# Kernel optimization log

Hardware: AMD Instinct MI355X
Metric: run time of the kernel (lower is better)

## Reference

```python
import jax, jax.numpy as jnp
import numpy as np

RES = 128        # 2**base_lod, base_lod=7, num_lod=1
FEAT_DIM = 18


def setup_inputs() -> dict:
    key = jax.random.key(0)
    k1, k2 = jax.random.split(key)
    pts = jax.random.uniform(k1, (4, 524288, 3), dtype=jnp.float32)
    codebook = jax.random.normal(k2, (RES ** 3, FEAT_DIM), dtype=jnp.float32) * 0.01
    transform = jnp.eye(4, dtype=jnp.float32)
    return {"pts": pts, "codebook": codebook, "transform": transform}


def _trilinear(res, codebook, pts):
    # pts: [N,3] in [0,1]; NGLOD-style dense grid trilinear interpolation
    p = pts * (res - 1)
    p0 = jnp.floor(p)
    w = p - p0                                   # [N,3] fractional weights
    i0 = jnp.clip(p0.astype(jnp.int32), 0, res - 1)
    i1 = jnp.clip(i0 + 1, 0, res - 1)
    feats = jnp.zeros((pts.shape[0], codebook.shape[1]), dtype=codebook.dtype)
    for dz in (0, 1):
        iz = (i1 if dz else i0)[:, 2]
        wz = w[:, 2] if dz else 1.0 - w[:, 2]
        for dy in (0, 1):
            iy = (i1 if dy else i0)[:, 1]
            wy = w[:, 1] if dy else 1.0 - w[:, 1]
            for dx in (0, 1):
                ix = (i1 if dx else i0)[:, 0]
                wx = w[:, 0] if dx else 1.0 - w[:, 0]
                idx = ix + iy * res + iz * res * res   # x + y*res + z*res^2
                feats = feats + codebook[idx] * (wx * wy * wz)[:, None]
    return feats


def reference(pts, codebook, transform):
    # flatten 'b h c -> (b h) c'
    p = pts.reshape(-1, 3)
    R_inv = jnp.linalg.inv(transform[:3, :3])
    p = (R_inv @ (p.T - transform[:3, 3:4])).T
    feats = _trilinear(RES, codebook, p)
    # single LOD: cat over lod axis then sum(-1) is identity
    return feats
```

## Files before the change

### kernel.cpp

```cpp
#include <hip/hip_runtime.h>


constexpr int RES = 128;
constexpr int NB  = 512;
constexpr int TPB = 576;
constexpr int PPB = TPB / 9;

constexpr int HIST_CHUNK = 1024;
constexpr int SCAT_CHUNK = 4096;

typedef float vf2 __attribute__((ext_vector_type(2)));
typedef float vf4 __attribute__((ext_vector_type(4)));

struct Xf {
    float m00, m01, m02, m10, m11, m12, m20, m21, m22;
    float tx, ty, tz;
};

__device__ __forceinline__ Xf load_xf(const float* __restrict__ tr) {
    Xf X;
    const float a = tr[0], b = tr[1],  c = tr[2];
    const float d = tr[4], e = tr[5],  g = tr[6];
    const float h = tr[8], i = tr[9],  j = tr[10];
    X.tx = tr[3]; X.ty = tr[7]; X.tz = tr[11];
    const float det = a*(e*j - g*i) - b*(d*j - g*h) + c*(d*i - e*h);
    const float rd  = 1.0f / det;
    X.m00 = (e*j - g*i) * rd; X.m01 = (c*i - b*j) * rd; X.m02 = (b*g - c*e) * rd;
    X.m10 = (g*h - d*j) * rd; X.m11 = (a*j - c*h) * rd; X.m12 = (c*d - a*g) * rd;
    X.m20 = (d*i - e*h) * rd; X.m21 = (b*h - a*i) * rd; X.m22 = (a*e - b*d) * rd;
    return X;
}

__device__ __forceinline__ float qcoord(float m0, float m1, float m2,
                                        float x, float y, float z) {
    return __fmaf_rn(m0, x, __fmaf_rn(m1, y, m2 * z)) * (float)(RES - 1);
}

__device__ __forceinline__ int bin_of(const Xf& X, float x, float y, float z) {
    const float qy = qcoord(X.m10, X.m11, X.m12, x, y, z);
    const float qz = qcoord(X.m20, X.m21, X.m22, x, y, z);
    const int iy0 = min(max((int)floorf(qy), 0), RES - 1);
    const int iz0 = min(max((int)floorf(qz), 0), RES - 1);
    return (iz0 << 2) + (iy0 >> 5);
}

__global__ __launch_bounds__(NB)
void k_zero(unsigned* __restrict__ hist) {
    hist[threadIdx.x] = 0u;
}

__global__ __launch_bounds__(256)
void k_hist(const float* __restrict__ pts, const float* __restrict__ tr,
            unsigned* __restrict__ hist, int npts)
{
    __shared__ unsigned sh[NB];
    for (int b = threadIdx.x; b < NB; b += 256) sh[b] = 0u;
    __syncthreads();
    const Xf X = load_xf(tr);
    const int base = blockIdx.x * HIST_CHUNK;
    #pragma unroll
    for (int i = 0; i < HIST_CHUNK / 256; ++i) {
        const int p = base + threadIdx.x + i * 256;
        if (p < npts) {
            const float x = pts[p*3 + 0] - X.tx;
            const float y = pts[p*3 + 1] - X.ty;
            const float z = pts[p*3 + 2] - X.tz;
            atomicAdd(&sh[bin_of(X, x, y, z)], 1u);
        }
    }
    __syncthreads();
    for (int b = threadIdx.x; b < NB; b += 256) {
        const unsigned c = sh[b];
        if (c) atomicAdd(&hist[b], c);
    }
}

__global__ __launch_bounds__(NB)
void k_scan(const unsigned* __restrict__ hist, unsigned* __restrict__ cursor)
{
    __shared__ unsigned s[NB];
    const int t = threadIdx.x;
    const unsigned my = hist[t];
    s[t] = my;
    __syncthreads();
    for (int off = 1; off < NB; off <<= 1) {
        const unsigned v = (t >= off) ? s[t - off] : 0u;
        __syncthreads();
        s[t] += v;
        __syncthreads();
    }
    cursor[t] = s[t] - my;
}

__global__ __launch_bounds__(256)
void k_scatter(const float* __restrict__ pts, const float* __restrict__ tr,
               unsigned* __restrict__ cursor, vf4* __restrict__ rec, int npts)
{
    __shared__ unsigned shist[NB], sbase[NB], scur[NB];
    const int t = threadIdx.x;
    for (int b = t; b < NB; b += 256) { shist[b] = 0u; scur[b] = 0u; }
    __syncthreads();
    const Xf X = load_xf(tr);
    const int base = blockIdx.x * SCAT_CHUNK;
    #pragma unroll
    for (int i = 0; i < SCAT_CHUNK / 256; ++i) {
        const int p = base + t + i * 256;
        if (p < npts) {
            const float x = pts[p*3 + 0] - X.tx;
            const float y = pts[p*3 + 1] - X.ty;
            const float z = pts[p*3 + 2] - X.tz;
            atomicAdd(&shist[bin_of(X, x, y, z)], 1u);
        }
    }
    __syncthreads();
    for (int b = t; b < NB; b += 256)
        sbase[b] = atomicAdd(&cursor[b], shist[b]);
    __syncthreads();
    #pragma unroll
    for (int i = 0; i < SCAT_CHUNK / 256; ++i) {
        const int p = base + t + i * 256;
        if (p < npts) {
            const float x = pts[p*3 + 0] - X.tx;
            const float y = pts[p*3 + 1] - X.ty;
            const float z = pts[p*3 + 2] - X.tz;
            const float qx = qcoord(X.m00, X.m01, X.m02, x, y, z);
            const float qy = qcoord(X.m10, X.m11, X.m12, x, y, z);
            const float qz = qcoord(X.m20, X.m21, X.m22, x, y, z);
            const int bn = bin_of(X, x, y, z);
            const unsigned r = atomicAdd(&scur[bn], 1u);
            unsigned pos = sbase[bn] + r;
            if (pos >= (unsigned)npts) pos = (unsigned)npts - 1u;
            vf4 v; v.x = qx; v.y = qy; v.z = qz; v.w = __int_as_float(p);
            rec[pos] = v;
        }
    }
}

__global__ __launch_bounds__(TPB)
void k_main(const vf4* __restrict__ rec, const float* __restrict__ cb,
            float* __restrict__ out, int npts)
{
    __shared__ vf4 srec[PPB];
    if (threadIdx.x < PPB) {
        const int g = blockIdx.x * PPB + threadIdx.x;
        if (g < npts) srec[threadIdx.x] = rec[g];
    }
    __syncthreads();

    const int pl = threadIdx.x / 9;
    const int f  = threadIdx.x - pl * 9;
    const int p  = blockIdx.x * PPB + pl;
    if (p >= npts) return;

    const vf4 r = srec[pl];
    const float qx = r.x, qy = r.y, qz = r.z;
    const int idx = __float_as_int(r.w);

    const float fx = floorf(qx), fy = floorf(qy), fz = floorf(qz);
    const float wx1 = qx - fx, wy1 = qy - fy, wz1 = qz - fz;
    const float wx0 = 1.0f - wx1, wy0 = 1.0f - wy1, wz0 = 1.0f - wz1;
    const int ix0 = min(max((int)fx, 0), RES - 1); const int ix1 = min(ix0 + 1, RES - 1);
    const int iy0 = min(max((int)fy, 0), RES - 1); const int iy1 = min(iy0 + 1, RES - 1);
    const int iz0 = min(max((int)fz, 0), RES - 1); const int iz1 = min(iz0 + 1, RES - 1);

    int   ro[8];
    float w[8];
    #pragma unroll
    for (int k = 0; k < 8; ++k) {
        const int dx = k & 1, dy = (k >> 1) & 1, dz = k >> 2;
        const int ix = dx ? ix1 : ix0;
        const int iy = dy ? iy1 : iy0;
        const int iz = dz ? iz1 : iz0;
        ro[k] = ix + (iy << 7) + (iz << 14);
        w[k]  = (dx ? wx1 : wx0) * (dy ? wy1 : wy0) * (dz ? wz1 : wz0);
    }

    const float* cbf = cb + 2 * f;
    vf2 v[8];
    #pragma unroll
    for (int k = 0; k < 8; ++k)
        v[k] = *reinterpret_cast<const vf2*>(cbf + ro[k] * 18);

    float ax = 0.0f, ay = 0.0f;
    #pragma unroll
    for (int k = 0; k < 8; ++k) { ax += v[k].x * w[k]; ay += v[k].y * w[k]; }

    vf2 o; o.x = ax; o.y = ay;
    __builtin_nontemporal_store(o, reinterpret_cast<vf2*>(out + idx * 18 + 2 * f));
}

__global__ __launch_bounds__(TPB)
void dense_grid_trilerp(const float* __restrict__ pts,
                        const float* __restrict__ cb,
                        const float* __restrict__ tr,
                        float* __restrict__ out,
                        int npts)
{
    __shared__ float spts[PPB * 3];
    if (threadIdx.x < PPB * 3) {
        int g = blockIdx.x * (PPB * 3) + threadIdx.x;
        spts[threadIdx.x] = (g < npts * 3) ? __builtin_nontemporal_load(&pts[g]) : 0.0f;
    }
    __syncthreads();

    const int pl = threadIdx.x / 9;
    const int f  = threadIdx.x - pl * 9;
    const int p  = blockIdx.x * PPB + pl;
    if (p >= npts) return;

    const Xf X = load_xf(tr);
    const float x = spts[pl*3 + 0] - X.tx;
    const float y = spts[pl*3 + 1] - X.ty;
    const float z = spts[pl*3 + 2] - X.tz;
    const float qx = qcoord(X.m00, X.m01, X.m02, x, y, z);
    const float qy = qcoord(X.m10, X.m11, X.m12, x, y, z);
    const float qz = qcoord(X.m20, X.m21, X.m22, x, y, z);

    const float fx = floorf(qx), fy = floorf(qy), fz = floorf(qz);
    const float wx1 = qx - fx, wy1 = qy - fy, wz1 = qz - fz;
    const float wx0 = 1.0f - wx1, wy0 = 1.0f - wy1, wz0 = 1.0f - wz1;
    const int ix0 = min(max((int)fx, 0), RES - 1); const int ix1 = min(ix0 + 1, RES - 1);
    const int iy0 = min(max((int)fy, 0), RES - 1); const int iy1 = min(iy0 + 1, RES - 1);
    const int iz0 = min(max((int)fz, 0), RES - 1); const int iz1 = min(iz0 + 1, RES - 1);

    int   ro[8];
    float w[8];
    #pragma unroll
    for (int k = 0; k < 8; ++k) {
        const int dx = k & 1, dy = (k >> 1) & 1, dz = k >> 2;
        const int ix = dx ? ix1 : ix0;
        const int iy = dy ? iy1 : iy0;
        const int iz = dz ? iz1 : iz0;
        ro[k] = ix + (iy << 7) + (iz << 14);
        w[k]  = (dx ? wx1 : wx0) * (dy ? wy1 : wy0) * (dz ? wz1 : wz0);
    }

    const float* cbf = cb + 2 * f;
    vf2 v[8];
    #pragma unroll
    for (int k = 0; k < 8; ++k)
        v[k] = *reinterpret_cast<const vf2*>(cbf + ro[k] * 18);

    float ax = 0.0f, ay = 0.0f;
    #pragma unroll
    for (int k = 0; k < 8; ++k) { ax += v[k].x * w[k]; ay += v[k].y * w[k]; }

    vf2 o; o.x = ax; o.y = ay;
    __builtin_nontemporal_store(o, reinterpret_cast<vf2*>(out + p * 18 + 2 * f));
}

extern "C" void kernel_launch(void* const* d_in, const int* in_sizes, int n_in,
                              void* d_out, int out_size, void* d_ws, size_t ws_size,
                              hipStream_t stream) {
    const float* pts = (const float*)d_in[0];
    const float* cb  = (const float*)d_in[1];
    const float* tr  = (const float*)d_in[2];
    float* out = (float*)d_out;

    const int npts = in_sizes[0] / 3;

    const size_t need = (size_t)NB * 2 * sizeof(unsigned) + (size_t)npts * 16 + 256;
    if (d_ws == nullptr || ws_size < need || npts <= 0) {
        const int blocks = (npts + PPB - 1) / PPB;
        dense_grid_trilerp<<<blocks, TPB, 0, stream>>>(pts, cb, tr, out, npts);
        return;
    }

    unsigned* hist   = (unsigned*)d_ws;
    unsigned* cursor = hist + NB;
    vf4* rec = (vf4*)((char*)d_ws + ((size_t)NB * 2 * sizeof(unsigned) + 255) / 256 * 256);

    k_zero<<<1, NB, 0, stream>>>(hist);
    k_hist<<<(npts + HIST_CHUNK - 1) / HIST_CHUNK, 256, 0, stream>>>(pts, tr, hist, npts);
    k_scan<<<1, NB, 0, stream>>>(hist, cursor);
    k_scatter<<<(npts + SCAT_CHUNK - 1) / SCAT_CHUNK, 256, 0, stream>>>(pts, tr, cursor, rec, npts);
    k_main<<<(npts + PPB - 1) / PPB, TPB, 0, stream>>>(rec, cb, out, npts);
}
```

Measured before the change: 506.5 us.

## Bin points per (y,z) row pair and stage codebook rows in LDS

Points are now sorted into 16384 bins, one per (iy0, iz0) cell column, using global atomics for the histogram and scatter instead of per-block shared-memory histograms. A multi-chunk single-block scan builds the bin offsets. The main kernel runs one block per bin and loads the four needed codebook x-rows (128 by 18 floats each) into LDS once. Each point's eight corner fetches are then served from LDS rather than from global memory. The costs are heavy contention on global atomics, a serial scan over 16K bins, and load imbalance, since each block copies about 37 KB of LDS for roughly 32 points on average.

```diff
diff --git a/kernel.cpp b/kernel.cpp
--- a/kernel.cpp
+++ b/kernel.cpp
@@ -2,12 +2,10 @@
 
 
 constexpr int RES = 128;
-constexpr int NB  = 512;
+constexpr int NB2 = 128 * 128;
 constexpr int TPB = 576;
 constexpr int PPB = TPB / 9;
-
-constexpr int HIST_CHUNK = 1024;
-constexpr int SCAT_CHUNK = 4096;
+constexpr int ROWF = 128 * 18;
 
 typedef float vf2 __attribute__((ext_vector_type(2)));
 typedef float vf4 __attribute__((ext_vector_type(4)));
@@ -36,114 +34,164 @@
     return __fmaf_rn(m0, x, __fmaf_rn(m1, y, m2 * z)) * (float)(RES - 1);
 }
 
-__device__ __forceinline__ int bin_of(const Xf& X, float x, float y, float z) {
-    const float qy = qcoord(X.m10, X.m11, X.m12, x, y, z);
-    const float qz = qcoord(X.m20, X.m21, X.m22, x, y, z);
+__device__ __forceinline__ int bin_of_qyz(float qy, float qz) {
     const int iy0 = min(max((int)floorf(qy), 0), RES - 1);
     const int iz0 = min(max((int)floorf(qz), 0), RES - 1);
-    return (iz0 << 2) + (iy0 >> 5);
-}
-
-__global__ __launch_bounds__(NB)
+    return (iz0 << 7) | iy0;
+}
+
+__global__ __launch_bounds__(256)
 void k_zero(unsigned* __restrict__ hist) {
-    hist[threadIdx.x] = 0u;
+    const int i = blockIdx.x * 256 + threadIdx.x;
+    if (i < NB2) hist[i] = 0u;
 }
 
 __global__ __launch_bounds__(256)
 void k_hist(const float* __restrict__ pts, const float* __restrict__ tr,
             unsigned* __restrict__ hist, int npts)
 {
-    __shared__ unsigned sh[NB];
-    for (int b = threadIdx.x; b < NB; b += 256) sh[b] = 0u;
-    __syncthreads();
+    const int p = blockIdx.x * 256 + threadIdx.x;
+    if (p >= npts) return;
     const Xf X = load_xf(tr);
-    const int base = blockIdx.x * HIST_CHUNK;
-    #pragma unroll
-    for (int i = 0; i < HIST_CHUNK / 256; ++i) {
-        const int p = base + threadIdx.x + i * 256;
-        if (p < npts) {
-            const float x = pts[p*3 + 0] - X.tx;
-            const float y = pts[p*3 + 1] - X.ty;
-            const float z = pts[p*3 + 2] - X.tz;
-            atomicAdd(&sh[bin_of(X, x, y, z)], 1u);
+    const float x = pts[p*3 + 0] - X.tx;
+    const float y = pts[p*3 + 1] - X.ty;
+    const float z = pts[p*3 + 2] - X.tz;
+    const float qy = qcoord(X.m10, X.m11, X.m12, x, y, z);
+    const float qz = qcoord(X.m20, X.m21, X.m22, x, y, z);
+    atomicAdd(&hist[bin_of_qyz(qy, qz)], 1u);
+}
+
+__global__ __launch_bounds__(1024)
+void k_scan(const unsigned* __restrict__ hist,
+            unsigned* __restrict__ base, unsigned* __restrict__ cursor)
+{
+    __shared__ unsigned s[1024];
+    const int t = threadIdx.x;
+    unsigned carry = 0u;
+    for (int c = 0; c < NB2 / 1024; ++c) {
+        const int i = c * 1024 + t;
+        const unsigned v = hist[i];
+        s[t] = v;
+        __syncthreads();
+        for (int off = 1; off < 1024; off <<= 1) {
+            const unsigned tmp = (t >= off) ? s[t - off] : 0u;
+            __syncthreads();
+            s[t] += tmp;
+            __syncthreads();
         }
-    }
-    __syncthreads();
-    for (int b = threadIdx.x; b < NB; b += 256) {
-        const unsigned c = sh[b];
-        if (c) atomicAdd(&hist[b], c);
-    }
-}
-
-__global__ __launch_bounds__(NB)
-void k_scan(const unsigned* __restrict__ hist, unsigned* __restrict__ cursor)
-{
-    __shared__ unsigned s[NB];
-    const int t = threadIdx.x;
-    const unsigned my = hist[t];
-    s[t] = my;
-    __syncthreads();
-    for (int off = 1; off < NB; off <<= 1) {
-        const unsigned v = (t >= off) ? s[t - off] : 0u;
-        __syncthreads();
-        s[t] += v;
-        __syncthreads();
-    }
-    cursor[t] = s[t] - my;
+        const unsigned excl = s[t] - v + carry;
+        base[i]   = excl;
+        cursor[i] = excl;
+        const unsigned tot = s[1023];
+        __syncthreads();
+        carry += tot;
+    }
 }
 
 __global__ __launch_bounds__(256)
 void k_scatter(const float* __restrict__ pts, const float* __restrict__ tr,
                unsigned* __restrict__ cursor, vf4* __restrict__ rec, int npts)
 {
-    __shared__ unsigned shist[NB], sbase[NB], scur[NB];
+    const int p = blockIdx.x * 256 + threadIdx.x;
+    if (p >= npts) return;
+    const Xf X = load_xf(tr);
+    const float x = pts[p*3 + 0] - X.tx;
+    const float y = pts[p*3 + 1] - X.ty;
+    const float z = pts[p*3 + 2] - X.tz;
+    const float qx = qcoord(X.m00, X.m01, X.m02, x, y, z);
+    const float qy = qcoord(X.m10, X.m11, X.m12, x, y, z);
+    const float qz = qcoord(X.m20, X.m21, X.m22, x, y, z);
+    const int bn = bin_of_qyz(qy, qz);
+    unsigned pos = atomicAdd(&cursor[bn], 1u);
+    if (pos >= (unsigned)npts) pos = (unsigned)npts - 1u;
+    vf4 v; v.x = qx; v.y = qy; v.z = qz; v.w = __int_as_float(p);
+    rec[pos] = v;
+}
+
+__global__ __launch_bounds__(TPB)
+void k_main(const vf4* __restrict__ rec, const unsigned* __restrict__ hist,
+            const unsigned* __restrict__ base, const float* __restrict__ cb,
+            float* __restrict__ out)
+{
+    const int b = blockIdx.x;
+    const unsigned n = hist[b];
+    if (n == 0u) return;
+    const unsigned bs = base[b];
+
+    const int iy0 = b & 127, iz0 = b >> 7;
+    const int iy1 = min(iy0 + 1, RES - 1), iz1 = min(iz0 + 1, RES - 1);
+
+    __shared__ float sld[4 * ROWF];
+    __shared__ vf4   srec[PPB];
+
     const int t = threadIdx.x;
-    for (int b = t; b < NB; b += 256) { shist[b] = 0u; scur[b] = 0u; }
-    __syncthreads();
-    const Xf X = load_xf(tr);
-    const int base = blockIdx.x * SCAT_CHUNK;
-    #pragma unroll
-    for (int i = 0; i < SCAT_CHUNK / 256; ++i) {
-        const int p = base + t + i * 256;
-        if (p < npts) {
-            const float x = pts[p*3 + 0] - X.tx;
-            const float y = pts[p*3 + 1] - X.ty;
-            const float z = pts[p*3 + 2] - X.tz;
-            atomicAdd(&shist[bin_of(X, x, y, z)], 1u);
+    {
+        const int ry[4] = { iy0, iy1, iy0, iy1 };
+        const int rz[4] = { iz0, iz0, iz1, iz1 };
+        #pragma unroll
+        for (int c = 0; c < 4; ++c) {
+            const vf4* src =
+                reinterpret_cast<const vf4*>(cb + (size_t)((rz[c] << 14) | (ry[c] << 7)) * 18);
+            reinterpret_cast<vf4*>(&sld[c * ROWF])[t] = src[t];
         }
     }
-    __syncthreads();
-    for (int b = t; b < NB; b += 256)
-        sbase[b] = atomicAdd(&cursor[b], shist[b]);
-    __syncthreads();
-    #pragma unroll
-    for (int i = 0; i < SCAT_CHUNK / 256; ++i) {
-        const int p = base + t + i * 256;
-        if (p < npts) {
-            const float x = pts[p*3 + 0] - X.tx;
-            const float y = pts[p*3 + 1] - X.ty;
-            const float z = pts[p*3 + 2] - X.tz;
-            const float qx = qcoord(X.m00, X.m01, X.m02, x, y, z);
-            const float qy = qcoord(X.m10, X.m11, X.m12, x, y, z);
-            const float qz = qcoord(X.m20, X.m21, X.m22, x, y, z);
-            const int bn = bin_of(X, x, y, z);
-            const unsigned r = atomicAdd(&scur[bn], 1u);
-            unsigned pos = sbase[bn] + r;
-            if (pos >= (unsigned)npts) pos = (unsigned)npts - 1u;
-            vf4 v; v.x = qx; v.y = qy; v.z = qz; v.w = __int_as_float(p);
-            rec[pos] = v;
+
+    const int pl = t / 9;
+    const int f  = t - pl * 9;
+
+    for (unsigned off = 0; off < n; off += PPB) {
+        __syncthreads();
+        if (t < PPB && off + (unsigned)t < n)
+            srec[t] = rec[bs + off + (unsigned)t];
+        __syncthreads();
+
+        if (off + (unsigned)pl < n) {
+            const vf4 r = srec[pl];
+            const float qx = r.x, qy = r.y, qz = r.z;
+            const int idx = __float_as_int(r.w);
+
+            const float fx = floorf(qx), fy = floorf(qy), fz = floorf(qz);
+            const float wx1 = qx - fx, wy1 = qy - fy, wz1 = qz - fz;
+            const float wx0 = 1.0f - wx1, wy0 = 1.0f - wy1, wz0 = 1.0f - wz1;
+            const int ix0 = min(max((int)fx, 0), RES - 1);
+            const int ix1 = min(ix0 + 1, RES - 1);
+
+            const int x18_0 = ix0 * 18 + 2 * f;
+            const int x18_1 = ix1 * 18 + 2 * f;
+
+            vf2   v[8];
+            float w[8];
+            #pragma unroll
+            for (int k = 0; k < 8; ++k) {
+                const int dx = k & 1, dy = (k >> 1) & 1, dz = k >> 2;
+                const int cell = dy + 2 * dz;
+                const int o = cell * ROWF + (dx ? x18_1 : x18_0);
+                v[k] = *reinterpret_cast<const vf2*>(&sld[o]);
+                w[k] = (dx ? wx1 : wx0) * (dy ? wy1 : wy0) * (dz ? wz1 : wz0);
+            }
+
+            float ax = 0.0f, ay = 0.0f;
+            #pragma unroll
+            for (int k = 0; k < 8; ++k) { ax += v[k].x * w[k]; ay += v[k].y * w[k]; }
+
+            vf2 o2; o2.x = ax; o2.y = ay;
+            __builtin_nontemporal_store(o2,
+                reinterpret_cast<vf2*>(out + (size_t)idx * 18 + 2 * f));
         }
     }
 }
 
 __global__ __launch_bounds__(TPB)
-void k_main(const vf4* __restrict__ rec, const float* __restrict__ cb,
-            float* __restrict__ out, int npts)
-{
-    __shared__ vf4 srec[PPB];
-    if (threadIdx.x < PPB) {
-        const int g = blockIdx.x * PPB + threadIdx.x;
-        if (g < npts) srec[threadIdx.x] = rec[g];
+void dense_grid_trilerp(const float* __restrict__ pts,
+                        const float* __restrict__ cb,
+                        const float* __restrict__ tr,
+                        float* __restrict__ out,
+                        int npts)
+{
+    __shared__ float spts[PPB * 3];
+    if (threadIdx.x < PPB * 3) {
+        int g = blockIdx.x * (PPB * 3) + threadIdx.x;
+        spts[threadIdx.x] = (g < npts * 3) ? __builtin_nontemporal_load(&pts[g]) : 0.0f;
     }
     __syncthreads();
 
@@ -152,9 +200,13 @@
     const int p  = blockIdx.x * PPB + pl;
     if (p >= npts) return;
 
-    const vf4 r = srec[pl];
-    const float qx = r.x, qy = r.y, qz = r.z;
-    const int idx = __float_as_int(r.w);
+    const Xf X = load_xf(tr);
+    const float x = spts[pl*3 + 0] - X.tx;
+    const float y = spts[pl*3 + 1] - X.ty;
+    const float z = spts[pl*3 + 2] - X.tz;
+    const float qx = qcoord(X.m00, X.m01, X.m02, x, y, z);
+    const float qy = qcoord(X.m10, X.m11, X.m12, x, y, z);
+    const float qz = qcoord(X.m20, X.m21, X.m22, x, y, z);
 
     const float fx = floorf(qx), fy = floorf(qy), fz = floorf(qz);
     const float wx1 = qx - fx, wy1 = qy - fy, wz1 = qz - fz;
@@ -186,66 +238,6 @@
     for (int k = 0; k < 8; ++k) { ax += v[k].x * w[k]; ay += v[k].y * w[k]; }
 
     vf2 o; o.x = ax; o.y = ay;
-    __builtin_nontemporal_store(o, reinterpret_cast<vf2*>(out + idx * 18 + 2 * f));
-}
-
-__global__ __launch_bounds__(TPB)
-void dense_grid_trilerp(const float* __restrict__ pts,
-                        const float* __restrict__ cb,
-                        const float* __restrict__ tr,
-                        float* __restrict__ out,
-                        int npts)
-{
-    __shared__ float spts[PPB * 3];
-    if (threadIdx.x < PPB * 3) {
-        int g = blockIdx.x * (PPB * 3) + threadIdx.x;
-        spts[threadIdx.x] = (g < npts * 3) ? __builtin_nontemporal_load(&pts[g]) : 0.0f;
-    }
-    __syncthreads();
-
-    const int pl = threadIdx.x / 9;
-    const int f  = threadIdx.x - pl * 9;
-    const int p  = blockIdx.x * PPB + pl;
-    if (p >= npts) return;
-
-    const Xf X = load_xf(tr);
-    const float x = spts[pl*3 + 0] - X.tx;
-    const float y = spts[pl*3 + 1] - X.ty;
-    const float z = spts[pl*3 + 2] - X.tz;
-    const float qx = qcoord(X.m00, X.m01, X.m02, x, y, z);
-    const float qy = qcoord(X.m10, X.m11, X.m12, x, y, z);
-    const float qz = qcoord(X.m20, X.m21, X.m22, x, y, z);
-
-    const float fx = floorf(qx), fy = floorf(qy), fz = floorf(qz);
-    const float wx1 = qx - fx, wy1 = qy - fy, wz1 = qz - fz;
-    const float wx0 = 1.0f - wx1, wy0 = 1.0f - wy1, wz0 = 1.0f - wz1;
-    const int ix0 = min(max((int)fx, 0), RES - 1); const int ix1 = min(ix0 + 1, RES - 1);
-    const int iy0 = min(max((int)fy, 0), RES - 1); const int iy1 = min(iy0 + 1, RES - 1);
-    const int iz0 = min(max((int)fz, 0), RES - 1); const int iz1 = min(iz0 + 1, RES - 1);
-
-    int   ro[8];
-    float w[8];
-    #pragma unroll
-    for (int k = 0; k < 8; ++k) {
-        const int dx = k & 1, dy = (k >> 1) & 1, dz = k >> 2;
-        const int ix = dx ? ix1 : ix0;
-        const int iy = dy ? iy1 : iy0;
-        const int iz = dz ? iz1 : iz0;
-        ro[k] = ix + (iy << 7) + (iz << 14);
-        w[k]  = (dx ? wx1 : wx0) * (dy ? wy1 : wy0) * (dz ? wz1 : wz0);
-    }
-
-    const float* cbf = cb + 2 * f;
-    vf2 v[8];
-    #pragma unroll
-    for (int k = 0; k < 8; ++k)
-        v[k] = *reinterpret_cast<const vf2*>(cbf + ro[k] * 18);
-
-    float ax = 0.0f, ay = 0.0f;
-    #pragma unroll
-    for (int k = 0; k < 8; ++k) { ax += v[k].x * w[k]; ay += v[k].y * w[k]; }
-
-    vf2 o; o.x = ax; o.y = ay;
     __builtin_nontemporal_store(o, reinterpret_cast<vf2*>(out + p * 18 + 2 * f));
 }
 
@@ -259,7 +251,8 @@
 
     const int npts = in_sizes[0] / 3;
 
-    const size_t need = (size_t)NB * 2 * sizeof(unsigned) + (size_t)npts * 16 + 256;
+    const size_t meta  = (size_t)NB2 * 3 * sizeof(unsigned);
+    const size_t need  = meta + (size_t)npts * 16 + 256;
     if (d_ws == nullptr || ws_size < need || npts <= 0) {
         const int blocks = (npts + PPB - 1) / PPB;
         dense_grid_trilerp<<<blocks, TPB, 0, stream>>>(pts, cb, tr, out, npts);
@@ -267,12 +260,14 @@
     }
 
     unsigned* hist   = (unsigned*)d_ws;
-    unsigned* cursor = hist + NB;
-    vf4* rec = (vf4*)((char*)d_ws + ((size_t)NB * 2 * sizeof(unsigned) + 255) / 256 * 256);
-
-    k_zero<<<1, NB, 0, stream>>>(hist);
-    k_hist<<<(npts + HIST_CHUNK - 1) / HIST_CHUNK, 256, 0, stream>>>(pts, tr, hist, npts);
-    k_scan<<<1, NB, 0, stream>>>(hist, cursor);
-    k_scatter<<<(npts + SCAT_CHUNK - 1) / SCAT_CHUNK, 256, 0, stream>>>(pts, tr, cursor, rec, npts);
-    k_main<<<(npts + PPB - 1) / PPB, TPB, 0, stream>>>(rec, cb, out, npts);
-}
+    unsigned* base   = hist + NB2;
+    unsigned* cursor = base + NB2;
+    vf4* rec = (vf4*)((char*)d_ws + ((meta + 255) / 256) * 256);
+
+    const int pblocks = (npts + 255) / 256;
+    k_zero<<<(NB2 + 255) / 256, 256, 0, stream>>>(hist);
+    k_hist<<<pblocks, 256, 0, stream>>>(pts, tr, hist, npts);
+    k_scan<<<1, 1024, 0, stream>>>(hist, base, cursor);
+    k_scatter<<<pblocks, 256, 0, stream>>>(pts, tr, cursor, rec, npts);
+    k_main<<<NB2, TPB, 0, stream>>>(rec, hist, base, cb, out);
+}
```

Result: slower. 629.5 us (+24.3%).

## Sub-sort points by y row and stage codebook rows in LDS per coarse bin

Applied to the files above, without the earlier changes.

Adds a per-coarse-bin subsort kernel that reorders the binned point records by their y row. The main kernel now runs one block per (z, y-group) bin and streams the needed codebook rows for z and z+1 into a 4-slot LDS ring, so the 8-corner lookups read LDS instead of gathering from global memory. This is meant to cut the scattered global codebook reads. In exchange it adds an extra read/write pass over the records, a large LDS footprint that limits occupancy, a barrier per y row, and a slow global-gather fallback for bins with more than 8160 points.

```diff
diff --git a/kernel.cpp b/kernel.cpp
--- a/kernel.cpp
+++ b/kernel.cpp
@@ -1,13 +1,15 @@
 #include <hip/hip_runtime.h>
 
 
-constexpr int RES = 128;
-constexpr int NB  = 512;
-constexpr int TPB = 576;
-constexpr int PPB = TPB / 9;
+constexpr int RES  = 128;
+constexpr int NBA  = 512;
+constexpr int TPM  = 576;
+constexpr int PPB  = 64;
+constexpr int ROWF = 128 * 18;
+constexpr int SUB_CAP = 8160;
 
 constexpr int HIST_CHUNK = 1024;
-constexpr int SCAT_CHUNK = 4096;
+constexpr int SCAT_CHUNK = 8192;
 
 typedef float vf2 __attribute__((ext_vector_type(2)));
 typedef float vf4 __attribute__((ext_vector_type(4)));
@@ -36,69 +38,75 @@
     return __fmaf_rn(m0, x, __fmaf_rn(m1, y, m2 * z)) * (float)(RES - 1);
 }
 
-__device__ __forceinline__ int bin_of(const Xf& X, float x, float y, float z) {
-    const float qy = qcoord(X.m10, X.m11, X.m12, x, y, z);
-    const float qz = qcoord(X.m20, X.m21, X.m22, x, y, z);
-    const int iy0 = min(max((int)floorf(qy), 0), RES - 1);
-    const int iz0 = min(max((int)floorf(qz), 0), RES - 1);
-    return (iz0 << 2) + (iy0 >> 5);
-}
-
-__global__ __launch_bounds__(NB)
-void k_zero(unsigned* __restrict__ hist) {
-    hist[threadIdx.x] = 0u;
+__device__ __forceinline__ int clamp_idx(float q) {
+    return min(max((int)floorf(q), 0), RES - 1);
+}
+
+__device__ __forceinline__ int coarse_key(float qy, float qz) {
+    return (clamp_idx(qz) << 2) | (clamp_idx(qy) >> 5);
 }
 
 __global__ __launch_bounds__(256)
-void k_hist(const float* __restrict__ pts, const float* __restrict__ tr,
-            unsigned* __restrict__ hist, int npts)
-{
-    __shared__ unsigned sh[NB];
-    for (int b = threadIdx.x; b < NB; b += 256) sh[b] = 0u;
+void k_zero(unsigned* __restrict__ histA) {
+    const int i = blockIdx.x * 256 + threadIdx.x;
+    if (i < NBA) histA[i] = 0u;
+}
+
+__global__ __launch_bounds__(256)
+void k_histA(const float* __restrict__ pts, const float* __restrict__ tr,
+             unsigned* __restrict__ histA, int npts)
+{
+    __shared__ unsigned sh[NBA];
+    const int t = threadIdx.x;
+    for (int b = t; b < NBA; b += 256) sh[b] = 0u;
     __syncthreads();
     const Xf X = load_xf(tr);
     const int base = blockIdx.x * HIST_CHUNK;
     #pragma unroll
     for (int i = 0; i < HIST_CHUNK / 256; ++i) {
-        const int p = base + threadIdx.x + i * 256;
+        const int p = base + t + i * 256;
         if (p < npts) {
             const float x = pts[p*3 + 0] - X.tx;
             const float y = pts[p*3 + 1] - X.ty;
             const float z = pts[p*3 + 2] - X.tz;
-            atomicAdd(&sh[bin_of(X, x, y, z)], 1u);
-        }
-    }
-    __syncthreads();
-    for (int b = threadIdx.x; b < NB; b += 256) {
+            const float qy = qcoord(X.m10, X.m11, X.m12, x, y, z);
+            const float qz = qcoord(X.m20, X.m21, X.m22, x, y, z);
+            atomicAdd(&sh[coarse_key(qy, qz)], 1u);
+        }
+    }
+    __syncthreads();
+    for (int b = t; b < NBA; b += 256) {
         const unsigned c = sh[b];
-        if (c) atomicAdd(&hist[b], c);
-    }
-}
-
-__global__ __launch_bounds__(NB)
-void k_scan(const unsigned* __restrict__ hist, unsigned* __restrict__ cursor)
-{
-    __shared__ unsigned s[NB];
-    const int t = threadIdx.x;
-    const unsigned my = hist[t];
+        if (c) atomicAdd(&histA[b], c);
+    }
+}
+
+__global__ __launch_bounds__(NBA)
+void k_scanA(const unsigned* __restrict__ histA,
+             unsigned* __restrict__ baseA, unsigned* __restrict__ cursorA)
+{
+    __shared__ unsigned s[NBA];
+    const int t = threadIdx.x;
+    const unsigned my = histA[t];
     s[t] = my;
     __syncthreads();
-    for (int off = 1; off < NB; off <<= 1) {
+    for (int off = 1; off < NBA; off <<= 1) {
         const unsigned v = (t >= off) ? s[t - off] : 0u;
         __syncthreads();
         s[t] += v;
         __syncthreads();
     }
-    cursor[t] = s[t] - my;
+    baseA[t]   = s[t] - my;
+    cursorA[t] = s[t] - my;
 }
 
 __global__ __launch_bounds__(256)
-void k_scatter(const float* __restrict__ pts, const float* __restrict__ tr,
-               unsigned* __restrict__ cursor, vf4* __restrict__ rec, int npts)
-{
-    __shared__ unsigned shist[NB], sbase[NB], scur[NB];
-    const int t = threadIdx.x;
-    for (int b = t; b < NB; b += 256) { shist[b] = 0u; scur[b] = 0u; }
+void k_scatA(const float* __restrict__ pts, const float* __restrict__ tr,
+             unsigned* __restrict__ cursorA, vf4* __restrict__ rec, int npts)
+{
+    __shared__ unsigned shist[NBA], sbase[NBA], scur[NBA];
+    const int t = threadIdx.x;
+    for (int b = t; b < NBA; b += 256) { shist[b] = 0u; scur[b] = 0u; }
     __syncthreads();
     const Xf X = load_xf(tr);
     const int base = blockIdx.x * SCAT_CHUNK;
@@ -109,12 +117,14 @@
             const float x = pts[p*3 + 0] - X.tx;
             const float y = pts[p*3 + 1] - X.ty;
             const float z = pts[p*3 + 2] - X.tz;
-            atomicAdd(&shist[bin_of(X, x, y, z)], 1u);
-        }
-    }
-    __syncthreads();
-    for (int b = t; b < NB; b += 256)
-        sbase[b] = atomicAdd(&cursor[b], shist[b]);
+            const float qy = qcoord(X.m10, X.m11, X.m12, x, y, z);
+            const float qz = qcoord(X.m20, X.m21, X.m22, x, y, z);
+            atomicAdd(&shist[coarse_key(qy, qz)], 1u);
+        }
+    }
+    __syncthreads();
+    for (int b = t; b < NBA; b += 256)
+        sbase[b] = shist[b] ? atomicAdd(&cursorA[b], shist[b]) : 0u;
     __syncthreads();
     #pragma unroll
     for (int i = 0; i < SCAT_CHUNK / 256; ++i) {
@@ -126,7 +136,7 @@
             const float qx = qcoord(X.m00, X.m01, X.m02, x, y, z);
             const float qy = qcoord(X.m10, X.m11, X.m12, x, y, z);
             const float qz = qcoord(X.m20, X.m21, X.m22, x, y, z);
-            const int bn = bin_of(X, x, y, z);
+            const int bn = coarse_key(qy, qz);
             const unsigned r = atomicAdd(&scur[bn], 1u);
             unsigned pos = sbase[bn] + r;
             if (pos >= (unsigned)npts) pos = (unsigned)npts - 1u;
@@ -136,60 +146,159 @@
     }
 }
 
-__global__ __launch_bounds__(TPB)
-void k_main(const vf4* __restrict__ rec, const float* __restrict__ cb,
-            float* __restrict__ out, int npts)
-{
-    __shared__ vf4 srec[PPB];
-    if (threadIdx.x < PPB) {
-        const int g = blockIdx.x * PPB + threadIdx.x;
-        if (g < npts) srec[threadIdx.x] = rec[g];
-    }
-    __syncthreads();
-
-    const int pl = threadIdx.x / 9;
-    const int f  = threadIdx.x - pl * 9;
-    const int p  = blockIdx.x * PPB + pl;
-    if (p >= npts) return;
-
-    const vf4 r = srec[pl];
-    const float qx = r.x, qy = r.y, qz = r.z;
-    const int idx = __float_as_int(r.w);
-
-    const float fx = floorf(qx), fy = floorf(qy), fz = floorf(qz);
-    const float wx1 = qx - fx, wy1 = qy - fy, wz1 = qz - fz;
-    const float wx0 = 1.0f - wx1, wy0 = 1.0f - wy1, wz0 = 1.0f - wz1;
-    const int ix0 = min(max((int)fx, 0), RES - 1); const int ix1 = min(ix0 + 1, RES - 1);
-    const int iy0 = min(max((int)fy, 0), RES - 1); const int iy1 = min(iy0 + 1, RES - 1);
-    const int iz0 = min(max((int)fz, 0), RES - 1); const int iz1 = min(iz0 + 1, RES - 1);
-
-    int   ro[8];
-    float w[8];
-    #pragma unroll
-    for (int k = 0; k < 8; ++k) {
-        const int dx = k & 1, dy = (k >> 1) & 1, dz = k >> 2;
-        const int ix = dx ? ix1 : ix0;
-        const int iy = dy ? iy1 : iy0;
-        const int iz = dz ? iz1 : iz0;
-        ro[k] = ix + (iy << 7) + (iz << 14);
-        w[k]  = (dx ? wx1 : wx0) * (dy ? wy1 : wy0) * (dz ? wz1 : wz0);
-    }
-
-    const float* cbf = cb + 2 * f;
-    vf2 v[8];
-    #pragma unroll
-    for (int k = 0; k < 8; ++k)
-        v[k] = *reinterpret_cast<const vf2*>(cbf + ro[k] * 18);
-
-    float ax = 0.0f, ay = 0.0f;
-    #pragma unroll
-    for (int k = 0; k < 8; ++k) { ax += v[k].x * w[k]; ay += v[k].y * w[k]; }
-
-    vf2 o; o.x = ax; o.y = ay;
-    __builtin_nontemporal_store(o, reinterpret_cast<vf2*>(out + idx * 18 + 2 * f));
-}
-
-__global__ __launch_bounds__(TPB)
+__global__ __launch_bounds__(1024)
+void k_subsort(vf4* __restrict__ rec, const unsigned* __restrict__ histA,
+               const unsigned* __restrict__ baseA, unsigned* __restrict__ histF)
+{
+    const int cbn = blockIdx.x;
+    const int t = threadIdx.x;
+    const unsigned n = histA[cbn];
+    const unsigned b0 = baseA[cbn];
+    const int iz0 = cbn >> 2;
+    const int ybase = (cbn & 3) << 5;
+    const int bf = (iz0 << 7) | ybase;
+
+    if (n == 0u) { if (t < 32) histF[bf + t] = 0u; return; }
+    if (n > (unsigned)SUB_CAP) {
+        if (t < 32) histF[bf + t] = (t == 0) ? (n | 0x80000000u) : 0u;
+        return;
+    }
+
+    __shared__ vf4 c[SUB_CAP];
+    __shared__ unsigned h[32], cur[32];
+    if (t < 32) h[t] = 0u;
+    __syncthreads();
+
+    for (unsigned i = t; i < n; i += 1024) {
+        const vf4 v = rec[b0 + i];
+        c[i] = v;
+        const int key = min(max(clamp_idx(v.y) - ybase, 0), 31);
+        atomicAdd(&h[key], 1u);
+    }
+    __syncthreads();
+    if (t == 0) {
+        unsigned run = 0u;
+        for (int k = 0; k < 32; ++k) { cur[k] = run; run += h[k]; }
+    }
+    __syncthreads();
+    for (unsigned i = t; i < n; i += 1024) {
+        const vf4 v = c[i];
+        const int key = min(max(clamp_idx(v.y) - ybase, 0), 31);
+        const unsigned pos = atomicAdd(&cur[key], 1u);
+        rec[b0 + pos] = v;
+    }
+    if (t < 32) histF[bf + t] = h[t];
+}
+
+__global__ __launch_bounds__(TPM)
+void k_main5(const vf4* __restrict__ rec, const unsigned* __restrict__ histF,
+             const unsigned* __restrict__ baseA, const float* __restrict__ cbk,
+             float* __restrict__ out)
+{
+    const int blk = blockIdx.x;
+    const int iz0 = blk >> 2;
+    const int ybase = (blk & 3) << 5;
+    const int t = threadIdx.x;
+    const int pl = t / 9;
+    const int f  = t - pl * 9;
+
+    __shared__ float sld[4][2][ROWF];
+
+    const unsigned bs = baseA[blk];
+    const unsigned nj0raw = histF[(iz0 << 7) | ybase];
+
+    auto stage = [&](int yn) {
+        const int yc = min(yn, RES - 1);
+        const int s  = yn & 3;
+        #pragma unroll
+        for (int zz = 0; zz < 2; ++zz) {
+            const int zc = min(iz0 + zz, RES - 1);
+            const vf2* __restrict__ src =
+                reinterpret_cast<const vf2*>(cbk + (size_t)((zc << 14) | (yc << 7)) * 18);
+            vf2* dst = reinterpret_cast<vf2*>(&sld[s][zz][0]);
+            dst[t]       = src[t];
+            dst[t + TPM] = src[t + TPM];
+        }
+    };
+
+    if (nj0raw & 0x80000000u) {
+        const unsigned n = nj0raw & 0x7fffffffu;
+        for (unsigned off = 0; off < n; off += PPB) {
+            const unsigned pi = off + (unsigned)pl;
+            if (pi < n) {
+                const vf4 r = rec[bs + pi];
+                const float qx = r.x, qy = r.y, qz = r.z;
+                const int idx = __float_as_int(r.w);
+                const float fx = floorf(qx), fy = floorf(qy), fz = floorf(qz);
+                const float wx1 = qx - fx, wy1 = qy - fy, wz1 = qz - fz;
+                const float wx0 = 1.0f - wx1, wy0 = 1.0f - wy1, wz0 = 1.0f - wz1;
+                const int ix0 = clamp_idx(qx), ix1 = min(ix0 + 1, RES - 1);
+                const int iy0 = clamp_idx(qy), iy1 = min(iy0 + 1, RES - 1);
+                const int izp = clamp_idx(qz), iz1 = min(izp + 1, RES - 1);
+                vf2 v[8]; float w[8];
+                #pragma unroll
+                for (int k = 0; k < 8; ++k) {
+                    const int dx = k & 1, dy = (k >> 1) & 1, dz = k >> 2;
+                    const int ro = (dx ? ix1 : ix0) + ((dy ? iy1 : iy0) << 7)
+                                 + ((dz ? iz1 : izp) << 14);
+                    v[k] = *reinterpret_cast<const vf2*>(cbk + (size_t)ro * 18 + 2 * f);
+                    w[k] = (dx ? wx1 : wx0) * (dy ? wy1 : wy0) * (dz ? wz1 : wz0);
+                }
+                float ax = 0.0f, ay = 0.0f;
+                #pragma unroll
+                for (int k = 0; k < 8; ++k) { ax += v[k].x * w[k]; ay += v[k].y * w[k]; }
+                vf2 o; o.x = ax; o.y = ay;
+                __builtin_nontemporal_store(o,
+                    reinterpret_cast<vf2*>(out + (size_t)idx * 18 + 2 * f));
+            }
+        }
+        return;
+    }
+
+    stage(ybase);
+    stage(ybase + 1);
+    unsigned cur = bs;
+    __syncthreads();
+
+    for (int j = 0; j < 32; ++j) {
+        const int iy0 = ybase + j;
+        const unsigned nj = histF[(iz0 << 7) | iy0];
+        if (j < 31) stage(iy0 + 2);
+
+        const int sy0 = iy0 & 3, sy1 = (iy0 + 1) & 3;
+        for (unsigned off = 0; off < nj; off += PPB) {
+            const unsigned pi = off + (unsigned)pl;
+            if (pi < nj) {
+                const vf4 r = __builtin_nontemporal_load(&rec[cur + pi]);
+                const float qx = r.x, qy = r.y, qz = r.z;
+                const int idx = __float_as_int(r.w);
+                const float fx = floorf(qx), fy = floorf(qy), fz = floorf(qz);
+                const float wx1 = qx - fx, wy1 = qy - fy, wz1 = qz - fz;
+                const float wx0 = 1.0f - wx1, wy0 = 1.0f - wy1, wz0 = 1.0f - wz1;
+                const int ix0 = clamp_idx(qx), ix1 = min(ix0 + 1, RES - 1);
+                const int x0 = ix0 * 18 + 2 * f, x1 = ix1 * 18 + 2 * f;
+                vf2 v[8]; float w[8];
+                #pragma unroll
+                for (int k = 0; k < 8; ++k) {
+                    const int dx = k & 1, dy = (k >> 1) & 1, dz = k >> 2;
+                    const float* base_ = &sld[dy ? sy1 : sy0][dz][0];
+                    v[k] = *reinterpret_cast<const vf2*>(&base_[dx ? x1 : x0]);
+                    w[k] = (dx ? wx1 : wx0) * (dy ? wy1 : wy0) * (dz ? wz1 : wz0);
+                }
+                float ax = 0.0f, ay = 0.0f;
+                #pragma unroll
+                for (int k = 0; k < 8; ++k) { ax += v[k].x * w[k]; ay += v[k].y * w[k]; }
+                vf2 o; o.x = ax; o.y = ay;
+                __builtin_nontemporal_store(o,
+                    reinterpret_cast<vf2*>(out + (size_t)idx * 18 + 2 * f));
+            }
+        }
+        cur += nj;
+        __syncthreads();
+    }
+}
+
+__global__ __launch_bounds__(TPM)
 void dense_grid_trilerp(const float* __restrict__ pts,
                         const float* __restrict__ cb,
                         const float* __restrict__ tr,
@@ -219,19 +328,16 @@
     const float fx = floorf(qx), fy = floorf(qy), fz = floorf(qz);
     const float wx1 = qx - fx, wy1 = qy - fy, wz1 = qz - fz;
     const float wx0 = 1.0f - wx1, wy0 = 1.0f - wy1, wz0 = 1.0f - wz1;
-    const int ix0 = min(max((int)fx, 0), RES - 1); const int ix1 = min(ix0 + 1, RES - 1);
-    const int iy0 = min(max((int)fy, 0), RES - 1); const int iy1 = min(iy0 + 1, RES - 1);
-    const int iz0 = min(max((int)fz, 0), RES - 1); const int iz1 = min(iz0 + 1, RES - 1);
+    const int ix0 = clamp_idx(qx); const int ix1 = min(ix0 + 1, RES - 1);
+    const int iy0 = clamp_idx(qy); const int iy1 = min(iy0 + 1, RES - 1);
+    const int iz0 = clamp_idx(qz); const int iz1 = min(iz0 + 1, RES - 1);
 
     int   ro[8];
     float w[8];
     #pragma unroll
     for (int k = 0; k < 8; ++k) {
         const int dx = k & 1, dy = (k >> 1) & 1, dz = k >> 2;
-        const int ix = dx ? ix1 : ix0;
-        const int iy = dy ? iy1 : iy0;
-        const int iz = dz ? iz1 : iz0;
-        ro[k] = ix + (iy << 7) + (iz << 14);
+        ro[k] = (dx ? ix1 : ix0) + ((dy ? iy1 : iy0) << 7) + ((dz ? iz1 : iz0) << 14);
         w[k]  = (dx ? wx1 : wx0) * (dy ? wy1 : wy0) * (dz ? wz1 : wz0);
     }
 
@@ -259,20 +365,24 @@
 
     const int npts = in_sizes[0] / 3;
 
-    const size_t need = (size_t)NB * 2 * sizeof(unsigned) + (size_t)npts * 16 + 256;
+    const size_t meta = (size_t)(NBA * 3 + 16384) * sizeof(unsigned);
+    const size_t need = meta + (size_t)npts * 16;
     if (d_ws == nullptr || ws_size < need || npts <= 0) {
         const int blocks = (npts + PPB - 1) / PPB;
-        dense_grid_trilerp<<<blocks, TPB, 0, stream>>>(pts, cb, tr, out, npts);
+        dense_grid_trilerp<<<blocks, TPM, 0, stream>>>(pts, cb, tr, out, npts);
         return;
     }
 
-    unsigned* hist   = (unsigned*)d_ws;
-    unsigned* cursor = hist + NB;
-    vf4* rec = (vf4*)((char*)d_ws + ((size_t)NB * 2 * sizeof(unsigned) + 255) / 256 * 256);
-
-    k_zero<<<1, NB, 0, stream>>>(hist);
-    k_hist<<<(npts + HIST_CHUNK - 1) / HIST_CHUNK, 256, 0, stream>>>(pts, tr, hist, npts);
-    k_scan<<<1, NB, 0, stream>>>(hist, cursor);
-    k_scatter<<<(npts + SCAT_CHUNK - 1) / SCAT_CHUNK, 256, 0, stream>>>(pts, tr, cursor, rec, npts);
-    k_main<<<(npts + PPB - 1) / PPB, TPB, 0, stream>>>(rec, cb, out, npts);
-}
+    unsigned* histA   = (unsigned*)d_ws;
+    unsigned* baseA   = histA + NBA;
+    unsigned* cursorA = baseA + NBA;
+    unsigned* histF   = cursorA + NBA;
+    vf4* rec = (vf4*)((char*)d_ws + meta);
+
+    k_zero<<<(NBA + 255) / 256, 256, 0, stream>>>(histA);
+    k_histA<<<(npts + HIST_CHUNK - 1) / HIST_CHUNK, 256, 0, stream>>>(pts, tr, histA, npts);
+    k_scanA<<<1, NBA, 0, stream>>>(histA, baseA, cursorA);
+    k_scatA<<<(npts + SCAT_CHUNK - 1) / SCAT_CHUNK, 256, 0, stream>>>(pts, tr, cursorA, rec, npts);
+    k_subsort<<<NBA, 1024, 0, stream>>>(rec, histA, baseA, histF);
+    k_main5<<<NBA, TPM, 0, stream>>>(rec, histF, baseA, cb, out);
+}
```

Result: no change. 506.6 us (+0.0%).
